# Kernel optimization log

Hardware: AMD Instinct MI355X
Metric: run time of the kernel (lower is better)

The kernel has to match this reference:

```python
import jax, jax.numpy as jnp
import numpy as np

EPS = 1e-8

def _matrix_sqrt(cov):
    # e @ diag(max(w,EPS))**0.5 @ e.T
    w, e = jnp.linalg.eigh(cov)
    w = jnp.maximum(w, EPS)
    return (e * jnp.sqrt(w)[None, :]) @ e.T

def _matrix_sqrt_neg(cov):
    # cov jittered on diagonal, then e @ diag(1/max(w,EPS))**0.5 @ e.T
    D = cov.shape[-1]
    cov = cov * (jnp.ones_like(cov) + jnp.eye(D, dtype=cov.dtype) * 0.001)
    w, e = jnp.linalg.eigh(cov)
    w = jnp.maximum(w, EPS)
    return (e * (1.0 / jnp.sqrt(w))[None, :]) @ e.T

def _match_axis(xc, R, mu, counter):
    # xc: (C, M, D) per-channel rows; R: (C, D, D) accumulated second moment; mu: (C, D)
    mu_test = xc.mean(1, keepdims=True)                      # (C,1,D)
    h = xc - mu_test                                         # centered test features
    cov_train = R / counter - mu[:, :, None] * mu[:, None, :]  # (C,D,D)
    sqrt_train = jax.vmap(_matrix_sqrt)(cov_train)           # (C,D,D)
    M = h.shape[1]
    cov_test = jnp.einsum('cmd,cme->cde', h, h) / M          # (C,D,D)
    neg_sqrt_test = jax.vmap(_matrix_sqrt_neg)(cov_test)     # (C,D,D)
    T = jnp.einsum('cde,cef->cdf', neg_sqrt_test, sqrt_train)  # whiten-then-recolor map
    return jnp.einsum('cmd,cdf->cmf', h, T) + mu[:, None, :]

def reference(x, cov_H, mu_H, cov_W, mu_W, counter):
    N, H, W, C = x.shape
    cnt = jnp.asarray(counter, dtype=x.dtype)
    # H-axis matching: rows of length H, per channel
    xh = x.transpose(3, 0, 2, 1).reshape(C, N * W, H)
    xh = _match_axis(xh, cov_H, mu_H, cnt)
    # W-axis matching: rows of length W, per channel
    xw = xh.reshape(C, N, W, H).transpose(0, 1, 3, 2).reshape(C, N * H, W)
    xw = _match_axis(xw, cov_W, mu_W, cnt)
    return xw.reshape(C, N, H, W).transpose(1, 2, 3, 0)

def setup_inputs() -> dict:
    key = jax.random.key(0)
    k1, k2, k3, k4, k5 = jax.random.split(key, 5)
    N, H, W, C = 64, 56, 56, 256
    counter = 716800  # accumulated sample count (N*W per acc batch)
    x = jax.random.normal(k1, (N, H, W, C), dtype=jnp.float32)
    mu_H = 0.1 * jax.random.normal(k2, (C, H), dtype=jnp.float32)
    mu_W = 0.1 * jax.random.normal(k3, (C, W), dtype=jnp.float32)
    # Build accumulated second moments so R/counter - outer(mu) is PSD
    BH = jax.random.normal(k4, (C, H, H), dtype=jnp.float32)
    SH = jnp.einsum('cij,ckj->cik', BH, BH) / H + 0.1 * jnp.eye(H, dtype=jnp.float32)
    cov_H = (SH + mu_H[:, :, None] * mu_H[:, None, :]) * counter
    BW = jax.random.normal(k5, (C, W, W), dtype=jnp.float32)
    SW = jnp.einsum('cij,ckj->cik', BW, BW) / W + 0.1 * jnp.eye(W, dtype=jnp.float32)
    cov_W = (SW + mu_W[:, :, None] * mu_W[:, None, :]) * counter
    return {"x": x, "cov_H": cov_H, "mu_H": mu_H, "cov_W": cov_W, "mu_W": mu_W, "counter": counter}
```

## Files before the change

### kernel.cpp

```cpp
#include <hip/hip_runtime.h>

#define C_ 256
#define D_ 56
#define N_ 64
#define M_ 3584
#define DD_ 3136
#define PL_ 200704
#define NS_ITERS 16

typedef __attribute__((ext_vector_type(8))) short v8s;
typedef __attribute__((ext_vector_type(8))) _Float16 v8h;
typedef __attribute__((ext_vector_type(4))) _Float16 v4h;
typedef __attribute__((ext_vector_type(4))) float v4f;

__device__ __forceinline__ unsigned short f2bf(float f) {
  union { float f; unsigned u; } x; x.f = f;
  unsigned r = x.u + 0x7FFFu + ((x.u >> 16) & 1u);
  return (unsigned short)(r >> 16);
}
__device__ __forceinline__ float bf2f(unsigned short h) {
  union { unsigned u; float f; } x; x.u = ((unsigned)h) << 16;
  return x.f;
}

__global__ __launch_bounds__(256) void k_tin(const float* __restrict__ x, _Float16* __restrict__ A) {
  int b = blockIdx.x;
  int cchunk = b & 3, g = b >> 2;
  int c0 = cchunk * 64;
  int m0 = g * 4;
  int n = m0 / 56, w0 = m0 % 56;
  __shared__ _Float16 t[4][56][66];
  int tid = threadIdx.x;
  const float4* x4 = (const float4*)x;
  #pragma unroll
  for (int it = 0; it < 14; ++it) {
    int i = tid + 256*it;
    int mloc = i / 896, r = i % 896;
    int h = r >> 4, cg = r & 15;
    float4 v = x4[((size_t)n*3136 + (size_t)h*56 + (w0+mloc))*64 + (c0>>2) + cg];
    t[mloc][h][4*cg+0] = (_Float16)v.x;
    t[mloc][h][4*cg+1] = (_Float16)v.y;
    t[mloc][h][4*cg+2] = (_Float16)v.z;
    t[mloc][h][4*cg+3] = (_Float16)v.w;
  }
  __syncthreads();
  #pragma unroll
  for (int it = 0; it < 7; ++it) {
    int j = tid + 256*it;
    int q = j / 7, hg = j % 7;
    int cc = q >> 2, mloc = q & 3;
    v8h o;
    #pragma unroll
    for (int k = 0; k < 8; ++k) o[k] = t[mloc][hg*8+k][cc];
    *(v8h*)&A[(size_t)(c0+cc)*PL_ + (size_t)(m0+mloc)*56 + hg*8] = o;
  }
}

__device__ __forceinline__ void mm_split_h(const _Float16 (*Ah)[72], const _Float16 (*Al)[72],
                                           const _Float16 (*Bh)[72], const _Float16 (*Bl)[72],
                                           int w, int lr, int lq, v4f (&acc)[4]) {
  v8h ah[2], al[2], bh[4][2], bl[4][2];
  #pragma unroll
  for (int s = 0; s < 2; ++s) {
    int kb = 32*s + 8*lq;
    ah[s] = *(const v8h*)&Ah[16*w + lr][kb];
    al[s] = *(const v8h*)&Al[16*w + lr][kb];
    #pragma unroll
    for (int jt = 0; jt < 4; ++jt) {
      bh[jt][s] = *(const v8h*)&Bh[16*jt + lr][kb];
      bl[jt][s] = *(const v8h*)&Bl[16*jt + lr][kb];
    }
  }
  #pragma unroll
  for (int jt = 0; jt < 4; ++jt) {
    #pragma unroll
    for (int s = 0; s < 2; ++s) {
      acc[jt] = __builtin_amdgcn_mfma_f32_16x16x32_f16(ah[s], bh[jt][s], acc[jt], 0, 0, 0);
      acc[jt] = __builtin_amdgcn_mfma_f32_16x16x32_f16(ah[s], bl[jt][s], acc[jt], 0, 0, 0);
      acc[jt] = __builtin_amdgcn_mfma_f32_16x16x32_f16(al[s], bh[jt][s], acc[jt], 0, 0, 0);
    }
  }
}

__device__ __forceinline__ void store_split_h(_Float16 (*H)[72], _Float16 (*L)[72],
                                              int w, int lr, int lq, const v4f (&val)[4]) {
  #pragma unroll
  for (int jt = 0; jt < 4; ++jt) {
    #pragma unroll
    for (int e = 0; e < 4; ++e) {
      int i = 16*w + 4*lq + e, j = 16*jt + lr;
      float v = val[jt][e];
      _Float16 h = (_Float16)v;
      H[i][j] = h;
      L[i][j] = (_Float16)(v - (float)h);
    }
  }
}

__global__ __launch_bounds__(256) void k_stats(const _Float16* __restrict__ in,
                                               float* __restrict__ muPart,
                                               float* __restrict__ covPart) {
  int b = blockIdx.x;
  int c = b >> 3, s = b & 7;
  const _Float16* p = in + (size_t)c*PL_ + (size_t)(s*448)*56;
  __shared__ __align__(16) char lds[18432];
  unsigned short (*At)[72]  = (unsigned short(*)[72])lds;
  unsigned short (*Alt)[72] = (unsigned short(*)[72])(lds + 9216);
  float (*Qbuf)[66] = (float(*)[66])lds;
  float (*red2)[60] = (float(*)[60])lds;
  int tid = threadIdx.x;
  int cg = tid % 7, rg = tid / 7;
  bool act = tid < 224;
  float cs[8] = {0.f,0.f,0.f,0.f,0.f,0.f,0.f,0.f};

  int l = tid & 63, w = tid >> 6;
  int lr = l & 15, lq = l >> 4;
  v4f zero4 = {0.f, 0.f, 0.f, 0.f};
  v4f accP[4], accQ[4];
  #pragma unroll
  for (int j = 0; j < 4; ++j) { accP[j] = zero4; accQ[j] = zero4; }

  v8h pre[2];
  if (act) {
    #pragma unroll
    for (int u = 0; u < 2; ++u)
      pre[u] = *(const v8h*)&p[(size_t)(rg + 32*u)*56 + cg*8];
  }
  for (int ch = 0; ch < 7; ++ch) {
    if (act) {
      #pragma unroll
      for (int u = 0; u < 2; ++u) {
        int m = rg + 32*u;
        v8h v = pre[u];
        #pragma unroll
        for (int k = 0; k < 8; ++k) {
          float f = (float)v[k];
          cs[k] += f;
          unsigned short h = f2bf(f);
          At[cg*8+k][m] = h;
          Alt[cg*8+k][m] = f2bf(f - bf2f(h));
        }
      }
    }
    __syncthreads();
    if (ch < 6 && act) {
      #pragma unroll
      for (int u = 0; u < 2; ++u)
        pre[u] = *(const v8h*)&p[(size_t)((ch+1)*64 + rg + 32*u)*56 + cg*8];
    }
    #pragma unroll
    for (int s2 = 0; s2 < 2; ++s2) {
      int kb = 32*s2 + 8*lq;
      v8s a = *(const v8s*)&At[16*w + lr][kb];
      #pragma unroll
      for (int j = 0; j < 4; ++j) {
        v8s bh = *(const v8s*)&At[16*j + lr][kb];
        v8s bl = *(const v8s*)&Alt[16*j + lr][kb];
        accP[j] = __builtin_amdgcn_mfma_f32_16x16x32_bf16(a, bh, accP[j], 0, 0, 0);
        accQ[j] = __builtin_amdgcn_mfma_f32_16x16x32_bf16(a, bl, accQ[j], 0, 0, 0);
      }
    }
    __syncthreads();
  }

  if (act) {
    #pragma unroll
    for (int k = 0; k < 8; ++k) red2[rg][cg*8+k] = cs[k];
  }
  __syncthreads();
  if (tid < 64) {
    float m = 0.f;
    if (tid < 56) {
      #pragma unroll
      for (int r = 0; r < 32; ++r) m += red2[r][tid];
    }
    muPart[((size_t)s*C_ + c)*64 + tid] = m;
  }
  __syncthreads();

  #pragma unroll
  for (int j = 0; j < 4; ++j) {
    #pragma unroll
    for (int e = 0; e < 4; ++e) {
      int r = 16*w + 4*lq + e, cc = 16*j + lr;
      Qbuf[r][cc] = accQ[j][e];
    }
  }
  __syncthreads();
  float* op = covPart + ((size_t)s*C_ + c)*DD_;
  #pragma unroll
  for (int j = 0; j < 4; ++j) {
    #pragma unroll
    for (int e = 0; e < 4; ++e) {
      int r = 16*w + 4*lq + e, cc = 16*j + lr;
      if (r < 56 && cc < 56) op[r*56 + cc] = accP[j][e] + accQ[j][e] + Qbuf[cc][r];
    }
  }
}

__global__ __launch_bounds__(256) void k_mured(const float* __restrict__ muPart, float* __restrict__ muT) {
  int idx = blockIdx.x*256 + threadIdx.x;
  if (idx >= C_*64) return;
  int c = idx >> 6, lane = idx & 63;
  float s = 0.f;
  for (int p = 0; p < 8; ++p) s += muPart[((size_t)p*C_ + c)*64 + lane];
  muT[idx] = s * (1.0f/M_);
}

__global__ __launch_bounds__(256) void k_finalize(const float* __restrict__ covPart, const float* __restrict__ muT,
                                                  const float* __restrict__ covIn, const float* __restrict__ muTrn,
                                                  const int* __restrict__ counter,
                                                  float* __restrict__ covTest, float* __restrict__ covTr) {
  int idx = blockIdx.x*256 + threadIdx.x;
  const int total = C_*DD_;
  if (idx < total) {
    int c = idx / DD_, r2 = idx % DD_, i = r2/56, j = r2%56;
    float ssum = 0.f;
    for (int s = 0; s < 8; ++s) ssum += covPart[((size_t)s*C_ + c)*DD_ + r2];
    float v = ssum*(1.0f/M_) - muT[c*64+i]*muT[c*64+j];
    if (i == j) v *= 1.001f;
    covTest[idx] = v;
  } else if (idx < 2*total) {
    int k = idx - total;
    int c = k / DD_, r2 = k % DD_, i = r2/56, j = r2%56;
    float cnt = (float)counter[0];
    covTr[k] = covIn[k]/cnt - muTrn[c*56+i]*muTrn[c*56+j];
  }
}

__global__ __launch_bounds__(256) void k_ns(const float* __restrict__ covTr, const float* __restrict__ covTest,
                                            float* __restrict__ Sout, float* __restrict__ Zout) {
  __shared__ __align__(16) _Float16 mats[6][64][72];
  __shared__ float red[4];
  int tid = threadIdx.x;
  int which = blockIdx.x & 1, c = blockIdx.x >> 1;
  const float4* Ain4 = (const float4*)((which ? covTest : covTr) + (size_t)c * DD_);

  typedef _Float16 (*mat_t)[72];
  mat_t Yh = mats[0], Yl = mats[1], Zh = mats[2], Zl = mats[3], Th = mats[4], Tl = mats[5];

  float ss = 0.f;
  for (int i4 = tid; i4 < 784; i4 += 256) {
    float4 v = Ain4[i4];
    ss += v.x*v.x + v.y*v.y + v.z*v.z + v.w*v.w;
  }
  { unsigned* z = (unsigned*)mats; for (int i = tid; i < 13824; i += 256) z[i] = 0u; }
  #pragma unroll
  for (int off = 32; off > 0; off >>= 1) ss += __shfl_down(ss, off, 64);
  if ((tid & 63) == 0) red[tid >> 6] = ss;
  __syncthreads();
  float s = sqrtf(red[0] + red[1] + red[2] + red[3]);
  float inv = 1.f / s;

  for (int i4 = tid; i4 < 784; i4 += 256) {
    float4 v = Ain4[i4];
    int r = i4 / 14, cgx = (i4 % 14) * 4;
    float f0 = v.x*inv, f1 = v.y*inv, f2 = v.z*inv, f3 = v.w*inv;
    v4h hh, ll;
    hh.x = (_Float16)f0; ll.x = (_Float16)(f0 - (float)hh.x);
    hh.y = (_Float16)f1; ll.y = (_Float16)(f1 - (float)hh.y);
    hh.z = (_Float16)f2; ll.z = (_Float16)(f2 - (float)hh.z);
    hh.w = (_Float16)f3; ll.w = (_Float16)(f3 - (float)hh.w);
    *(v4h*)&Yh[r][cgx] = hh;
    *(v4h*)&Yl[r][cgx] = ll;
  }
  if (tid < 56) Zh[tid][tid] = (_Float16)1.0f;
  __syncthreads();

  int lane = tid & 63, w = tid >> 6, lr = lane & 15, lq = lane >> 4;
  v4f zero4 = {0.f, 0.f, 0.f, 0.f};
  float rs = sqrtf(s);
  float fac = which ? (1.f/rs) : rs;
  float* outp = (which ? Zout : Sout) + (size_t)c*DD_;

  for (int it = 0; it < NS_ITERS; ++it) {
    v4f accW[4] = {zero4, zero4, zero4, zero4};
    mm_split_h(Zh, Zl, Yh, Yl, w, lr, lq, accW);
    v4f Tv[4];
    #pragma unroll
    for (int jt = 0; jt < 4; ++jt) {
      #pragma unroll
      for (int e = 0; e < 4; ++e) {
        float dv = (16*w + 4*lq + e == 16*jt + lr) ? 1.5f : 0.f;
        Tv[jt][e] = dv - 0.5f*accW[jt][e];
      }
    }
    store_split_h(Th, Tl, w, lr, lq, Tv);
    __syncthreads();
    if (it == NS_ITERS - 1) {
      v4f accF[4] = {zero4, zero4, zero4, zero4};
      if (which == 0) mm_split_h(Yh, Yl, Th, Tl, w, lr, lq, accF);
      else            mm_split_h(Th, Tl, Zh, Zl, w, lr, lq, accF);
      #pragma unroll
      for (int jt = 0; jt < 4; ++jt) {
        #pragma unroll
        for (int e = 0; e < 4; ++e) {
          int i = 16*w + 4*lq + e, j = 16*jt + lr;
          if (i < 56 && j < 56) outp[i*56 + j] = accF[jt][e] * fac;
        }
      }
    } else {
      v4f accY[4] = {zero4, zero4, zero4, zero4};
      v4f accZ[4] = {zero4, zero4, zero4, zero4};
      mm_split_h(Yh, Yl, Th, Tl, w, lr, lq, accY);
      mm_split_h(Th, Tl, Zh, Zl, w, lr, lq, accZ);
      __syncthreads();
      store_split_h(Yh, Yl, w, lr, lq, accY);
      store_split_h(Zh, Zl, w, lr, lq, accZ);
      __syncthreads();
    }
  }
}

__global__ __launch_bounds__(256) void k_tmap(const float* __restrict__ Zi, const float* __restrict__ Sm,
                                              float* __restrict__ Tm) {
  __shared__ __align__(16) _Float16 mats[4][64][72];
  int c = blockIdx.x, tid = threadIdx.x;
  typedef _Float16 (*mat_t)[72];
  mat_t Ah = mats[0], Al = mats[1], Bh = mats[2], Bl = mats[3];
  { unsigned* z = (unsigned*)mats; for (int i = tid; i < 9216; i += 256) z[i] = 0u; }
  __syncthreads();
  const float4* Z4 = (const float4*)(Zi + (size_t)c*DD_);
  const float4* S4 = (const float4*)(Sm + (size_t)c*DD_);
  for (int i4 = tid; i4 < 784; i4 += 256) {
    int r = i4 / 14, cgx = (i4 % 14) * 4;
    float4 v = Z4[i4];
    v4h hh, ll;
    hh.x = (_Float16)v.x; ll.x = (_Float16)(v.x - (float)hh.x);
    hh.y = (_Float16)v.y; ll.y = (_Float16)(v.y - (float)hh.y);
    hh.z = (_Float16)v.z; ll.z = (_Float16)(v.z - (float)hh.z);
    hh.w = (_Float16)v.w; ll.w = (_Float16)(v.w - (float)hh.w);
    *(v4h*)&Ah[r][cgx] = hh;
    *(v4h*)&Al[r][cgx] = ll;
    v = S4[i4];
    hh.x = (_Float16)v.x; ll.x = (_Float16)(v.x - (float)hh.x);
    hh.y = (_Float16)v.y; ll.y = (_Float16)(v.y - (float)hh.y);
    hh.z = (_Float16)v.z; ll.z = (_Float16)(v.z - (float)hh.z);
    hh.w = (_Float16)v.w; ll.w = (_Float16)(v.w - (float)hh.w);
    *(v4h*)&Bh[r][cgx] = hh;
    *(v4h*)&Bl[r][cgx] = ll;
  }
  __syncthreads();
  int lane = tid & 63, w = tid >> 6, lr = lane & 15, lq = lane >> 4;
  v4f zero4 = {0.f, 0.f, 0.f, 0.f};
  v4f acc[4] = {zero4, zero4, zero4, zero4};
  mm_split_h(Ah, Al, Bh, Bl, w, lr, lq, acc);
  float* op = Tm + (size_t)c*DD_;
  #pragma unroll
  for (int jt = 0; jt < 4; ++jt) {
    #pragma unroll
    for (int e = 0; e < 4; ++e) {
      int i = 16*w + 4*lq + e, j = 16*jt + lr;
      if (i < 56 && j < 56) op[i*56 + j] = acc[jt][e];
    }
  }
}

__global__ __launch_bounds__(256) void k_apply(const _Float16* __restrict__ in, const float* __restrict__ muT,
                                               const float* __restrict__ Tmp, const float* __restrict__ muTrain,
                                               _Float16* __restrict__ out, int stage) {
  int b = blockIdx.x;
  int c = b >> 4, ng = b & 15;
  int n0 = ng * 4;
  __shared__ __align__(16) _Float16 Abf[64][72];
  __shared__ __align__(16) _Float16 Tt[64][72];
  __shared__ float Y[56][57];
  __shared__ float smu[64], smt[64];
  int tid = threadIdx.x;
  if (tid < 64) {
    smu[tid] = muT[c*64 + tid];
    smt[tid] = (tid < 56) ? muTrain[c*56 + tid] : 0.f;
  }
  if (tid < 128) {
    int row = tid & 63;
    _Float16 (*Mz)[72] = (tid < 64) ? Abf : Tt;
    *(float4*)&Mz[row][56] = make_float4(0.f, 0.f, 0.f, 0.f);
  }
  const float4* t4 = (const float4*)(Tmp + (size_t)c*DD_);
  for (int i = tid; i < 784; i += 256) {
    float4 t = t4[i];
    int row = i / 14, cgx = (i % 14) * 4;
    Tt[cgx+0][row] = (_Float16)t.x;
    Tt[cgx+1][row] = (_Float16)t.y;
    Tt[cgx+2][row] = (_Float16)t.z;
    Tt[cgx+3][row] = (_Float16)t.w;
  }
  int l = tid & 63, w = tid >> 6;
  int lr = l & 15, lq = l >> 4;
  v4f zero4 = {0.f, 0.f, 0.f, 0.f};
  const v8h* p8base = (const v8h*)(in + (size_t)c*PL_);

  v8h preA[2], preB[2];
  {
    const v8h* p8 = p8base + (size_t)n0*392;
    #pragma unroll
    for (int u = 0; u < 2; ++u) { int i = tid + 256*u; if (i < 392) preA[u] = p8[i]; }
  }
  for (int t = 0; t < 4; ++t) {
    #pragma unroll
    for (int u = 0; u < 2; ++u) {
      int i = tid + 256*u;
      if (i < 392) {
        int row = i / 7, cg = i % 7;
        v8h pk;
        #pragma unroll
        for (int k = 0; k < 8; ++k) pk[k] = (_Float16)((float)preA[u][k] - smu[cg*8+k]);
        *(v8h*)&Abf[row][cg*8] = pk;
      }
    }
    __syncthreads();
    if (t < 3) {
      const v8h* p8 = p8base + (size_t)(n0+t+1)*392;
      #pragma unroll
      for (int u = 0; u < 2; ++u) { int i = tid + 256*u; if (i < 392) preB[u] = p8[i]; }
    }
    v4f acc[4] = {zero4, zero4, zero4, zero4};
    #pragma unroll
    for (int s = 0; s < 2; ++s) {
      int kb = 32*s + 8*lq;
      v8h a = *(const v8h*)&Abf[16*w + lr][kb];
      #pragma unroll
      for (int j = 0; j < 4; ++j) {
        v8h bb = *(const v8h*)&Tt[16*j + lr][kb];
        acc[j] = __builtin_amdgcn_mfma_f32_16x16x32_f16(a, bb, acc[j], 0, 0, 0);
      }
    }
    __syncthreads();
    #pragma unroll
    for (int j = 0; j < 4; ++j) {
      #pragma unroll
      for (int e = 0; e < 4; ++e) {
        int r = 16*w + 4*lq + e, cc = 16*j + lr;
        if (r < 56 && cc < 56) Y[r][cc] = acc[j][e] + smt[cc];
      }
    }
    __syncthreads();
    _Float16* o16 = out + (size_t)c*PL_ + (size_t)(n0+t)*3136;
    if (stage == 1) {
      for (int i = tid; i < 392; i += 256) {
        int h = i / 7, wg = i % 7;
        v8h o;
        #pragma unroll
        for (int k = 0; k < 8; ++k) o[k] = (_Float16)Y[wg*8+k][h];
        *(v8h*)&o16[h*56 + wg*8] = o;
      }
    } else {
      for (int i = tid; i < 392; i += 256) {
        int h = i / 7, wg = i % 7;
        v8h o;
        #pragma unroll
        for (int k = 0; k < 8; ++k) o[k] = (_Float16)Y[h][wg*8+k];
        *(v8h*)&o16[h*56 + wg*8] = o;
      }
    }
    preA[0] = preB[0]; preA[1] = preB[1];
  }
}

__global__ __launch_bounds__(256) void k_tout(const _Float16* __restrict__ A2, float* __restrict__ out) {
  int b = blockIdx.x;
  int cchunk = b & 3, g = b >> 2;
  int c0 = cchunk * 64;
  int nh0 = g * 4;
  __shared__ _Float16 t[4][56][66];
  int tid = threadIdx.x;
  #pragma unroll
  for (int it = 0; it < 7; ++it) {
    int j = tid + 256*it;
    int q = j / 7, wg = j % 7;
    int cc = q >> 2, mloc = q & 3;
    v8h v = *(const v8h*)&A2[(size_t)(c0+cc)*PL_ + (size_t)(nh0+mloc)*56 + wg*8];
    #pragma unroll
    for (int k = 0; k < 8; ++k) t[mloc][wg*8+k][cc] = v[k];
  }
  __syncthreads();
  float4* o4 = (float4*)out;
  #pragma unroll
  for (int it = 0; it < 14; ++it) {
    int i = tid + 256*it;
    int mloc = i / 896, r = i % 896;
    int w = r >> 4, cg = r & 15;
    float4 o;
    o.x = (float)t[mloc][w][4*cg+0];
    o.y = (float)t[mloc][w][4*cg+1];
    o.z = (float)t[mloc][w][4*cg+2];
    o.w = (float)t[mloc][w][4*cg+3];
    o4[((size_t)(nh0+mloc)*56 + w)*64 + (c0>>2) + cg] = o;
  }
}

extern "C" void kernel_launch(void* const* d_in, const int* in_sizes, int n_in,
                              void* d_out, int out_size, void* d_ws, size_t ws_size,
                              hipStream_t stream) {
  (void)in_sizes; (void)n_in; (void)out_size;
  const float* x    = (const float*)d_in[0];
  const float* covH = (const float*)d_in[1];
  const float* muH  = (const float*)d_in[2];
  const float* covW = (const float*)d_in[3];
  const float* muW  = (const float*)d_in[4];
  const int*   cnt  = (const int*)d_in[5];
  float* out = (float*)d_out;

  char* ws = (char*)d_ws;
  size_t off = 0;
  auto allocB = [&](size_t nbytes) {
    void* p = ws + off;
    off += ((nbytes + 255) / 256) * 256;
    return p;
  };
  _Float16* A16a  = (_Float16*)allocB((size_t)C_ * PL_ * 2);
  _Float16* A16b  = (_Float16*)allocB((size_t)C_ * PL_ * 2);
  float* covPart  = (float*)allocB((size_t)8 * C_ * DD_ * 4);
  float* muPart   = (float*)allocB((size_t)8 * C_ * 64 * 4);
  float* covTest  = (float*)allocB((size_t)C_ * DD_ * 4);
  float* covTr    = (float*)allocB((size_t)C_ * DD_ * 4);
  float* Sm       = (float*)allocB((size_t)C_ * DD_ * 4);
  float* Zim      = (float*)allocB((size_t)C_ * DD_ * 4);
  float* Tm       = (float*)allocB((size_t)C_ * DD_ * 4);
  float* muT      = (float*)allocB((size_t)C_ * 64 * 4);
  if (off > ws_size) return;

  dim3 blk(256);
  const int finGrid = (2*C_*DD_ + 255)/256;

  k_tin<<<dim3(4 * (M_/4)), blk, 0, stream>>>(x, A16a);

  k_stats   <<<dim3(2048),  blk, 0, stream>>>(A16a, muPart, covPart);
  k_mured   <<<dim3(64),    blk, 0, stream>>>(muPart, muT);
  k_finalize<<<dim3(finGrid), blk, 0, stream>>>(covPart, muT, covH, muH, cnt, covTest, covTr);
  k_ns      <<<dim3(512),   blk, 0, stream>>>(covTr, covTest, Sm, Zim);
  k_tmap    <<<dim3(256),   blk, 0, stream>>>(Zim, Sm, Tm);
  k_apply   <<<dim3(4096),  blk, 0, stream>>>(A16a, muT, Tm, muH, A16b, 1);

  k_stats   <<<dim3(2048),  blk, 0, stream>>>(A16b, muPart, covPart);
  k_mured   <<<dim3(64),    blk, 0, stream>>>(muPart, muT);
  k_finalize<<<dim3(finGrid), blk, 0, stream>>>(covPart, muT, covW, muW, cnt, covTest, covTr);
  k_ns      <<<dim3(512),   blk, 0, stream>>>(covTr, covTest, Sm, Zim);
  k_tmap    <<<dim3(256),   blk, 0, stream>>>(Zim, Sm, Tm);
  k_apply   <<<dim3(4096),  blk, 0, stream>>>(A16b, muT, Tm, muW, A16a, 2);

  k_tout<<<dim3(4 * (M_/4)), blk, 0, stream>>>(A16a, out);
}
```

Baseline: 491.4 us.

## Fuse mean/covariance finalize into Newton-Schulz kernel and halve stats partial splits

Removes the k_mured and k_finalize launches by having each k_ns block reduce the partial sums, subtract the mean outer product, apply the diagonal jitter and build the training covariance directly into shared memory. k_stats now runs 1024 blocks, each covering 896 rows instead of 448, so only 4 partials per channel are written and read. This cuts four kernel launches and the global round trips for covTest and covTr. In exchange k_stats has half as many blocks and a longer serial loop, and the shared-memory zeroing in k_ns is reduced to leave room for the raw matrix buffer.

New measurement: 473.0 us. 3.7% less time.

```diff
diff --git a/kernel.cpp b/kernel.cpp
--- a/kernel.cpp
+++ b/kernel.cpp
@@ -101,8 +101,8 @@
                                                float* __restrict__ muPart,
                                                float* __restrict__ covPart) {
   int b = blockIdx.x;
-  int c = b >> 3, s = b & 7;
-  const _Float16* p = in + (size_t)c*PL_ + (size_t)(s*448)*56;
+  int c = b >> 2, s = b & 3;
+  const _Float16* p = in + (size_t)c*PL_ + (size_t)(s*896)*56;
   __shared__ __align__(16) char lds[18432];
   unsigned short (*At)[72]  = (unsigned short(*)[72])lds;
   unsigned short (*Alt)[72] = (unsigned short(*)[72])(lds + 9216);
@@ -126,7 +126,7 @@
     for (int u = 0; u < 2; ++u)
       pre[u] = *(const v8h*)&p[(size_t)(rg + 32*u)*56 + cg*8];
   }
-  for (int ch = 0; ch < 7; ++ch) {
+  for (int ch = 0; ch < 14; ++ch) {
     if (act) {
       #pragma unroll
       for (int u = 0; u < 2; ++u) {
@@ -143,7 +143,7 @@
       }
     }
     __syncthreads();
-    if (ch < 6 && act) {
+    if (ch < 13 && act) {
       #pragma unroll
       for (int u = 0; u < 2; ++u)
         pre[u] = *(const v8h*)&p[(size_t)((ch+1)*64 + rg + 32*u)*56 + cg*8];
@@ -198,53 +198,72 @@
   }
 }
 
-__global__ __launch_bounds__(256) void k_mured(const float* __restrict__ muPart, float* __restrict__ muT) {
-  int idx = blockIdx.x*256 + threadIdx.x;
-  if (idx >= C_*64) return;
-  int c = idx >> 6, lane = idx & 63;
-  float s = 0.f;
-  for (int p = 0; p < 8; ++p) s += muPart[((size_t)p*C_ + c)*64 + lane];
-  muT[idx] = s * (1.0f/M_);
-}
-
-__global__ __launch_bounds__(256) void k_finalize(const float* __restrict__ covPart, const float* __restrict__ muT,
-                                                  const float* __restrict__ covIn, const float* __restrict__ muTrn,
-                                                  const int* __restrict__ counter,
-                                                  float* __restrict__ covTest, float* __restrict__ covTr) {
-  int idx = blockIdx.x*256 + threadIdx.x;
-  const int total = C_*DD_;
-  if (idx < total) {
-    int c = idx / DD_, r2 = idx % DD_, i = r2/56, j = r2%56;
-    float ssum = 0.f;
-    for (int s = 0; s < 8; ++s) ssum += covPart[((size_t)s*C_ + c)*DD_ + r2];
-    float v = ssum*(1.0f/M_) - muT[c*64+i]*muT[c*64+j];
-    if (i == j) v *= 1.001f;
-    covTest[idx] = v;
-  } else if (idx < 2*total) {
-    int k = idx - total;
-    int c = k / DD_, r2 = k % DD_, i = r2/56, j = r2%56;
-    float cnt = (float)counter[0];
-    covTr[k] = covIn[k]/cnt - muTrn[c*56+i]*muTrn[c*56+j];
-  }
-}
-
-__global__ __launch_bounds__(256) void k_ns(const float* __restrict__ covTr, const float* __restrict__ covTest,
-                                            float* __restrict__ Sout, float* __restrict__ Zout) {
+__global__ __launch_bounds__(256) void k_ns(const float* __restrict__ covIn, const float* __restrict__ muTrn,
+                                            const int* __restrict__ counter,
+                                            const float* __restrict__ covPart, const float* __restrict__ muPart,
+                                            float* __restrict__ Sout, float* __restrict__ Zout,
+                                            float* __restrict__ muT) {
   __shared__ __align__(16) _Float16 mats[6][64][72];
   __shared__ float red[4];
+  __shared__ float smu[64];
   int tid = threadIdx.x;
   int which = blockIdx.x & 1, c = blockIdx.x >> 1;
-  const float4* Ain4 = (const float4*)((which ? covTest : covTr) + (size_t)c * DD_);
-
   typedef _Float16 (*mat_t)[72];
   mat_t Yh = mats[0], Yl = mats[1], Zh = mats[2], Zl = mats[3], Th = mats[4], Tl = mats[5];
+  float (*Araw)[60] = (float(*)[60])&mats[4][0][0];
+
+  { unsigned* z = (unsigned*)mats; for (int i = tid; i < 9216; i += 256) z[i] = 0u; }
+
+  if (which == 0) {
+    if (tid < 64) smu[tid] = (tid < 56) ? muTrn[c*56 + tid] : 0.f;
+    __syncthreads();
+    float icnt = 1.f / (float)counter[0];
+    const float4* ci4 = (const float4*)(covIn + (size_t)c*DD_);
+    for (int i4 = tid; i4 < 784; i4 += 256) {
+      float4 v = ci4[i4];
+      int r = i4 / 14, cg = (i4 % 14) * 4;
+      float mr = smu[r];
+      v.x = v.x*icnt - mr*smu[cg+0];
+      v.y = v.y*icnt - mr*smu[cg+1];
+      v.z = v.z*icnt - mr*smu[cg+2];
+      v.w = v.w*icnt - mr*smu[cg+3];
+      *(float4*)&Araw[r][cg] = v;
+    }
+  } else {
+    if (tid < 64) {
+      float m = 0.f;
+      #pragma unroll
+      for (int p2 = 0; p2 < 4; ++p2) m += muPart[((size_t)p2*C_ + c)*64 + tid];
+      m *= (1.0f/M_);
+      smu[tid] = m;
+      muT[c*64 + tid] = m;
+    }
+    __syncthreads();
+    const float4* cp4 = (const float4*)covPart;
+    for (int i4 = tid; i4 < 784; i4 += 256) {
+      float4 a = make_float4(0.f, 0.f, 0.f, 0.f);
+      #pragma unroll
+      for (int p2 = 0; p2 < 4; ++p2) {
+        float4 v = cp4[((size_t)p2*C_ + c)*784 + i4];
+        a.x += v.x; a.y += v.y; a.z += v.z; a.w += v.w;
+      }
+      int r = i4 / 14, cg = (i4 % 14) * 4;
+      float mr = smu[r];
+      a.x = a.x*(1.0f/M_) - mr*smu[cg+0];
+      a.y = a.y*(1.0f/M_) - mr*smu[cg+1];
+      a.z = a.z*(1.0f/M_) - mr*smu[cg+2];
+      a.w = a.w*(1.0f/M_) - mr*smu[cg+3];
+      if (r == cg+0) a.x *= 1.001f;
+      if (r == cg+1) a.y *= 1.001f;
+      if (r == cg+2) a.z *= 1.001f;
+      if (r == cg+3) a.w *= 1.001f;
+      *(float4*)&Araw[r][cg] = a;
+    }
+  }
+  __syncthreads();
 
   float ss = 0.f;
-  for (int i4 = tid; i4 < 784; i4 += 256) {
-    float4 v = Ain4[i4];
-    ss += v.x*v.x + v.y*v.y + v.z*v.z + v.w*v.w;
-  }
-  { unsigned* z = (unsigned*)mats; for (int i = tid; i < 13824; i += 256) z[i] = 0u; }
+  for (int i = tid; i < DD_; i += 256) { float v = Araw[i/56][i%56]; ss += v*v; }
   #pragma unroll
   for (int off = 32; off > 0; off >>= 1) ss += __shfl_down(ss, off, 64);
   if ((tid & 63) == 0) red[tid >> 6] = ss;
@@ -253,8 +272,8 @@
   float inv = 1.f / s;
 
   for (int i4 = tid; i4 < 784; i4 += 256) {
-    float4 v = Ain4[i4];
     int r = i4 / 14, cgx = (i4 % 14) * 4;
+    float4 v = *(const float4*)&Araw[r][cgx];
     float f0 = v.x*inv, f1 = v.y*inv, f2 = v.z*inv, f3 = v.w*inv;
     v4h hh, ll;
     hh.x = (_Float16)f0; ll.x = (_Float16)(f0 - (float)hh.x);
@@ -510,10 +529,8 @@
   };
   _Float16* A16a  = (_Float16*)allocB((size_t)C_ * PL_ * 2);
   _Float16* A16b  = (_Float16*)allocB((size_t)C_ * PL_ * 2);
-  float* covPart  = (float*)allocB((size_t)8 * C_ * DD_ * 4);
-  float* muPart   = (float*)allocB((size_t)8 * C_ * 64 * 4);
-  float* covTest  = (float*)allocB((size_t)C_ * DD_ * 4);
-  float* covTr    = (float*)allocB((size_t)C_ * DD_ * 4);
+  float* covPart  = (float*)allocB((size_t)4 * C_ * DD_ * 4);
+  float* muPart   = (float*)allocB((size_t)4 * C_ * 64 * 4);
   float* Sm       = (float*)allocB((size_t)C_ * DD_ * 4);
   float* Zim      = (float*)allocB((size_t)C_ * DD_ * 4);
   float* Tm       = (float*)allocB((size_t)C_ * DD_ * 4);
@@ -521,23 +538,18 @@
   if (off > ws_size) return;
 
   dim3 blk(256);
-  const int finGrid = (2*C_*DD_ + 255)/256;
 
   k_tin<<<dim3(4 * (M_/4)), blk, 0, stream>>>(x, A16a);
 
-  k_stats   <<<dim3(2048),  blk, 0, stream>>>(A16a, muPart, covPart);
-  k_mured   <<<dim3(64),    blk, 0, stream>>>(muPart, muT);
-  k_finalize<<<dim3(finGrid), blk, 0, stream>>>(covPart, muT, covH, muH, cnt, covTest, covTr);
-  k_ns      <<<dim3(512),   blk, 0, stream>>>(covTr, covTest, Sm, Zim);
-  k_tmap    <<<dim3(256),   blk, 0, stream>>>(Zim, Sm, Tm);
-  k_apply   <<<dim3(4096),  blk, 0, stream>>>(A16a, muT, Tm, muH, A16b, 1);
-
-  k_stats   <<<dim3(2048),  blk, 0, stream>>>(A16b, muPart, covPart);
-  k_mured   <<<dim3(64),    blk, 0, stream>>>(muPart, muT);
-  k_finalize<<<dim3(finGrid), blk, 0, stream>>>(covPart, muT, covW, muW, cnt, covTest, covTr);
-  k_ns      <<<dim3(512),   blk, 0, stream>>>(covTr, covTest, Sm, Zim);
-  k_tmap    <<<dim3(256),   blk, 0, stream>>>(Zim, Sm, Tm);
-  k_apply   <<<dim3(4096),  blk, 0, stream>>>(A16b, muT, Tm, muW, A16a, 2);
+  k_stats<<<dim3(1024), blk, 0, stream>>>(A16a, muPart, covPart);
+  k_ns   <<<dim3(512),  blk, 0, stream>>>(covH, muH, cnt, covPart, muPart, Sm, Zim, muT);
+  k_tmap <<<dim3(256),  blk, 0, stream>>>(Zim, Sm, Tm);
+  k_apply<<<dim3(4096), blk, 0, stream>>>(A16a, muT, Tm, muH, A16b, 1);
+
+  k_stats<<<dim3(1024), blk, 0, stream>>>(A16b, muPart, covPart);
+  k_ns   <<<dim3(512),  blk, 0, stream>>>(covW, muW, cnt, covPart, muPart, Sm, Zim, muT);
+  k_tmap <<<dim3(256),  blk, 0, stream>>>(Zim, Sm, Tm);
+  k_apply<<<dim3(4096), blk, 0, stream>>>(A16b, muT, Tm, muW, A16a, 2);
 
   k_tout<<<dim3(4 * (M_/4)), blk, 0, stream>>>(A16a, out);
 }
```
